# Performance work log

Measured on AMD Instinct MI355X. Metric: run time of the kernel, lower is better.

## Reference

```python
import jax, jax.numpy as jnp
import numpy as np

N = 50000
E = 800000
C_IN = 32
C_OUT = 32
K = 8  # number of branch MLPs


def setup_inputs() -> dict:
    key = jax.random.key(0)
    ks = jax.random.split(key, 12)
    x = jax.random.normal(ks[0], (N, C_IN), dtype=jnp.float32)
    pos = jax.random.normal(ks[1], (N, 2), dtype=jnp.float32)
    edge_index = jax.random.randint(ks[2], (2, E), 0, N, dtype=jnp.int32)
    edge_attr = jax.random.normal(ks[3], (E, 4), dtype=jnp.float32)
    edge_weight = jax.random.uniform(ks[4], (E,), dtype=jnp.float32)
    s1 = 1.0 / np.sqrt(C_IN + 4)
    s2 = 1.0 / np.sqrt(C_OUT)
    W1 = jax.random.uniform(ks[5], (K, C_IN + 4, C_OUT), jnp.float32, -s1, s1)
    b1 = jax.random.uniform(ks[6], (K, C_OUT), jnp.float32, -s1, s1)
    W2 = jax.random.uniform(ks[7], (K, C_OUT, C_OUT), jnp.float32, -s2, s2)
    b2 = jax.random.uniform(ks[8], (K, C_OUT), jnp.float32, -s2, s2)
    sr = 1.0 / np.sqrt(C_IN)
    Wr = jax.random.uniform(ks[9], (C_IN, C_OUT), jnp.float32, -sr, sr)
    br = jax.random.uniform(ks[10], (C_OUT,), jnp.float32, -sr, sr)
    return {"x": x, "pos": pos, "edge_index": edge_index, "edge_attr": edge_attr,
            "edge_weight": edge_weight, "W1": W1, "b1": b1, "W2": W2, "b2": b2,
            "Wr": Wr, "br": br}


def reference(x, pos, edge_index, edge_attr, edge_weight, W1, b1, W2, b2, Wr, br):
    src = edge_index[0]  # j (source / neighbor)
    tgt = edge_index[1]  # i (target / aggregation index)

    # gather per-edge features
    x_i = x[tgt]                      # [E, C_IN]
    x_j = x[src]                      # [E, C_IN]
    diff = pos[src] - pos[tgt]        # [E, 2]

    # geometric branch index in [0, 8)
    con0 = (diff[:, 0] > 0).astype(jnp.int32)
    con1 = (diff[:, 1] > 0).astype(jnp.int32)
    con2 = (jnp.abs(diff[:, 0]) - jnp.abs(diff[:, 1]) > 0).astype(jnp.int32)
    idx = con0 + con1 * 2 + con2 * 4  # [E]

    m = jnp.concatenate([x_j - x_i, edge_attr], axis=1)  # [E, C_IN+4]
    # all 8 branch MLPs (Linear->ReLU->Linear->ReLU), then select per edge
    h = jax.nn.relu(jnp.einsum('ec,kcf->ekf', m, W1) + b1[None])   # [E, K, C_OUT]
    f_all = jax.nn.relu(jnp.einsum('ekf,kfg->ekg', h, W2) + b2[None])
    f = jnp.take_along_axis(f_all, idx[:, None, None], axis=1)[:, 0, :]  # [E, C_OUT]
    f = edge_weight[:, None] * f

    # scatter-mean over target nodes
    seg_sum = jax.ops.segment_sum(f, tgt, num_segments=N)
    counts = jax.ops.segment_sum(jnp.ones((f.shape[0],), f.dtype), tgt, num_segments=N)
    out = seg_sum / jnp.maximum(counts, 1.0)[:, None]

    # skip connection
    out = out + x @ Wr + br
    return out
```

## Files before the change

kernel.cpp:

```cpp
#include <hip/hip_runtime.h>

#define N_NODES 50000
#define N_EDGES 800000
#define K_BR    8
#define BCAP    131072
#define MLP_SLOTS (K_BR * BCAP)
#define SCAN_BLOCKS 196

typedef _Float16 h2 __attribute__((ext_vector_type(2)));
typedef _Float16 half8 __attribute__((ext_vector_type(8)));
typedef float f32x4 __attribute__((ext_vector_type(4)));

#define MFMA(a, b, c) __builtin_amdgcn_mfma_f32_16x16x32_f16((a), (b), (c), 0, 0, 0)

#define VAL_MASK 0x3FFFFFFFu
#define FLG_A    0x40000000u
#define FLG_P    0x80000000u


__device__ __forceinline__ int branch_idx(float dx, float dy) {
    return (dx > 0.0f ? 1 : 0) + (dy > 0.0f ? 2 : 0) +
           ((fabsf(dx) - fabsf(dy)) > 0.0f ? 4 : 0);
}

__device__ __forceinline__ unsigned int pk_bf16(float a, float b) {
    unsigned int ua = __float_as_uint(a), ub = __float_as_uint(b);
    ua += 0x7FFFu + ((ua >> 16) & 1u);
    ub += 0x7FFFu + ((ub >> 16) & 1u);
    return (ua >> 16) | (ub & 0xFFFF0000u);
}

__device__ __forceinline__ unsigned pk_f16pair(float a, float b) {
    h2 p; p.x = (_Float16)a; p.y = (_Float16)b;
    return __builtin_bit_cast(unsigned, p);
}

__device__ __forceinline__ unsigned short f16bits(float a) {
    _Float16 h = (_Float16)a;
    return __builtin_bit_cast(unsigned short, h);
}

__global__ void prep_kernel(const float* __restrict__ W1, const float* __restrict__ W2,
                            const float* __restrict__ x,
                            uint4* __restrict__ w1f4, uint4* __restrict__ w2f4,
                            unsigned* __restrict__ xh) {
    int t = blockIdx.x * 256 + threadIdx.x;
    if (t < 2048) {
        int L = t & 63, fl = t >> 6;
        int nt = fl & 1, kt = (fl >> 1) & 1, k = fl >> 2;
        int quad = L >> 4, col = L & 15;
        unsigned dw[4];
#pragma unroll
        for (int i = 0; i < 4; ++i) {
            float v0 = 0.0f, v1 = 0.0f;
            int k0 = kt * 32 + quad * 8 + 2 * i;
            if (k0 < 36)     v0 = W1[k * 1152 + k0 * 32 + nt * 16 + col];
            if (k0 + 1 < 36) v1 = W1[k * 1152 + (k0 + 1) * 32 + nt * 16 + col];
            dw[i] = pk_f16pair(v0, v1);
        }
        w1f4[t] = make_uint4(dw[0], dw[1], dw[2], dw[3]);
    } else if (t < 3072) {
        int u2 = t - 2048;
        int L = u2 & 63, fl = u2 >> 6;
        int nt = fl & 1, k = fl >> 1;
        int quad = L >> 4, col = L & 15;
        unsigned dw[4];
#pragma unroll
        for (int i = 0; i < 4; ++i) {
            int k0 = quad * 8 + 2 * i;
            dw[i] = pk_f16pair(W2[k * 1024 + k0 * 32 + nt * 16 + col],
                               W2[k * 1024 + (k0 + 1) * 32 + nt * 16 + col]);
        }
        w2f4[u2] = make_uint4(dw[0], dw[1], dw[2], dw[3]);
    }
#pragma unroll
    for (int rep = 0; rep < 2; ++rep) {
        int j = t + rep * 409600;
        if (j < 800000) {
            float2 xv = ((const float2*)x)[j];
            xh[j] = pk_bf16(xv.x, xv.y);
        }
    }
}

__global__ void pass1_kernel(const int* __restrict__ ei, const float* __restrict__ pos,
                             const float* __restrict__ ea, const float* __restrict__ ew,
                             int* __restrict__ cnt, int* __restrict__ bucketCur,
                             uint4* __restrict__ payload) {
    __shared__ int h[K_BR];
    __shared__ int base[K_BR];
    int t = threadIdx.x;
    if (t < K_BR) h[t] = 0;
    __syncthreads();
    int e = blockIdx.x * 256 + t;
    int s = ei[e], d = ei[N_EDGES + e];
    float2 ps = ((const float2*)pos)[s];
    float2 pd = ((const float2*)pos)[d];
    int k = branch_idx(ps.x - pd.x, ps.y - pd.y);
    int rank = atomicAdd(&h[k], 1);
    int slotLocal = atomicAdd(&cnt[d], 1);
    float4 eav = ((const float4*)ea)[e];
    unsigned ewh = (unsigned)f16bits(ew[e]);
    __syncthreads();
    if (t < K_BR) base[t] = (h[t] > 0) ? atomicAdd(&bucketCur[t], h[t]) : 0;
    __syncthreads();
    int idx = (k << 17) + base[k] + rank;
    payload[idx] = make_uint4((unsigned)s | ((unsigned)d << 16),
                              (unsigned)slotLocal | (ewh << 16),
                              pk_f16pair(eav.x, eav.y),
                              pk_f16pair(eav.z, eav.w));
}

__global__ void scan_kernel(const int* __restrict__ cnt, unsigned* __restrict__ ps,
                            int* __restrict__ nodeStart) {
    __shared__ int s[256];
    __shared__ int sh_off;
    int t = threadIdx.x, b = blockIdx.x;
    int i = b * 256 + t;
    int v = (i < N_NODES) ? cnt[i] : 0;
    s[t] = v;
    __syncthreads();
#pragma unroll
    for (int off = 1; off < 256; off <<= 1) {
        int tmp = (t >= off) ? s[t - off] : 0;
        __syncthreads();
        s[t] += tmp;
        __syncthreads();
    }
    int excl = s[t] - v;
    if (t == 255)
        atomicExch(&ps[b], (unsigned)s[255] | (b == 0 ? FLG_P : FLG_A));
    if (t == 0) sh_off = 0;
    if (t < 64 && b > 0) {
        int off = 0;
        int base = b - 1;
        for (;;) {
            int idx = base - t;
            unsigned w = 0;
            if (idx >= 0) {
                do { w = atomicOr(&ps[idx], 0u); } while (!(w & (FLG_A | FLG_P)));
            }
            bool isP = (w & FLG_P) != 0;
            unsigned long long pm = __ballot(isP);
            int firstP = pm ? (__ffsll((unsigned long long)pm) - 1) : 64;
            int contrib = (idx >= 0 && t <= firstP) ? (int)(w & VAL_MASK) : 0;
#pragma unroll
            for (int sh = 32; sh > 0; sh >>= 1) contrib += __shfl_down(contrib, sh, 64);
            contrib = __shfl(contrib, 0, 64);
            off += contrib;
            if (firstP < 64 || base - 64 < 0) break;
            base -= 64;
        }
        if (t == 0) sh_off = off;
    }
    __syncthreads();
    if (i < N_NODES) nodeStart[i] = excl + sh_off;
}

__global__ void __launch_bounds__(128) mlp_kernel(
    const uint4* __restrict__ payload,
    const unsigned* __restrict__ xh,
    const uint4* __restrict__ w1f4, const float* __restrict__ b1,
    const uint4* __restrict__ w2f4, const float* __restrict__ b2,
    const int* __restrict__ nodeStart,
    const int* __restrict__ bucketFill,
    unsigned short* __restrict__ fbuf) {
    __shared__ uint4 lds4[1312];
    char* lds = (char*)lds4;

    int t = blockIdx.x * 128 + threadIdx.x;
    int u = __builtin_amdgcn_readfirstlane(t);
    int k = u >> 17;
    int fill = bucketFill[k];
    if ((u & (BCAP - 1)) >= fill) return;
    int rel = t & (BCAP - 1);
    bool valid = rel < fill;
    int idx = (k << 17) + min(rel, fill - 1);

    int L = threadIdx.x & 63;
    int wv = threadIdx.x >> 6;
    char* mreg = lds + wv * 10496;
    char* hreg = mreg + 9216;
    int quad = L >> 4, col = L & 15;

    uint4 pl = payload[idx];
    int s = (int)(pl.x & 0xFFFFu);
    int d = (int)(pl.x >> 16);
    float w = (float)__builtin_bit_cast(_Float16, (unsigned short)(pl.y >> 16));
    int slot = valid ? (nodeStart[d] + (int)(pl.y & 0xFFFFu)) : 0;

    unsigned mw[16];
    const uint4* xj = ((const uint4*)xh) + 4 * (size_t)s;
    const uint4* xi = ((const uint4*)xh) + 4 * (size_t)d;
#pragma unroll
    for (int q = 0; q < 4; ++q) {
        uint4 a4 = xj[q], b4 = xi[q];
#pragma unroll
        for (int c = 0; c < 4; ++c) {
            unsigned ua = (&a4.x)[c], ub = (&b4.x)[c];
            float d0 = __uint_as_float(ua << 16) - __uint_as_float(ub << 16);
            float d1 = __uint_as_float(ua & 0xFFFF0000u) - __uint_as_float(ub & 0xFFFF0000u);
            mw[4 * q + c] = pk_f16pair(d0, d1);
        }
    }

    uint4* mrow = (uint4*)(mreg + L * 144);
    mrow[0] = make_uint4(mw[0], mw[1], mw[2], mw[3]);
    mrow[1] = make_uint4(mw[4], mw[5], mw[6], mw[7]);
    mrow[2] = make_uint4(mw[8], mw[9], mw[10], mw[11]);
    mrow[3] = make_uint4(mw[12], mw[13], mw[14], mw[15]);
    mrow[4] = make_uint4(pl.z, pl.w, 0u, 0u);
    mrow[5] = make_uint4(0u, 0u, 0u, 0u);
    mrow[6] = make_uint4(0u, 0u, 0u, 0u);
    mrow[7] = make_uint4(0u, 0u, 0u, 0u);

    half8 B1[2][2], B2[2];
#pragma unroll
    for (int kt = 0; kt < 2; ++kt)
#pragma unroll
        for (int nt = 0; nt < 2; ++nt)
            B1[kt][nt] = __builtin_bit_cast(half8, w1f4[((k * 2 + kt) * 2 + nt) * 64 + L]);
#pragma unroll
    for (int nt = 0; nt < 2; ++nt)
        B2[nt] = __builtin_bit_cast(half8, w2f4[(k * 2 + nt) * 64 + L]);
    float b1o0 = b1[k * 32 + col],      b1o1 = b1[k * 32 + 16 + col];
    float b2o0 = b2[k * 32 + col],      b2o1 = b2[k * 32 + 16 + col];

#pragma unroll
    for (int mt = 0; mt < 4; ++mt) {
        int arow = mt * 16 + col;
        half8 a0 = __builtin_bit_cast(half8, *(const uint4*)(mreg + arow * 144 + quad * 16));
        half8 a1 = __builtin_bit_cast(half8, *(const uint4*)(mreg + arow * 144 + 64 + quad * 16));
        f32x4 c0 = {b1o0, b1o0, b1o0, b1o0};
        f32x4 c1 = {b1o1, b1o1, b1o1, b1o1};
        c0 = MFMA(a0, B1[0][0], c0);
        c0 = MFMA(a1, B1[1][0], c0);
        c1 = MFMA(a0, B1[0][1], c1);
        c1 = MFMA(a1, B1[1][1], c1);
#pragma unroll
        for (int r = 0; r < 4; ++r) {
            int er = quad * 4 + r;
            *(unsigned short*)(hreg + er * 80 + col * 2)        = f16bits(fmaxf(c0[r], 0.0f));
            *(unsigned short*)(hreg + er * 80 + (16 + col) * 2) = f16bits(fmaxf(c1[r], 0.0f));
        }
        half8 ah = __builtin_bit_cast(half8, *(const uint4*)(hreg + col * 80 + quad * 16));
        f32x4 d0 = {b2o0, b2o0, b2o0, b2o0};
        f32x4 d1 = {b2o1, b2o1, b2o1, b2o1};
        d0 = MFMA(ah, B2[0], d0);
        d1 = MFMA(ah, B2[1], d1);
#pragma unroll
        for (int r = 0; r < 4; ++r) {
            int edge = mt * 16 + quad * 4 + r;
            *(unsigned short*)(mreg + edge * 144 + col * 2)        = f16bits(fmaxf(d0[r], 0.0f));
            *(unsigned short*)(mreg + edge * 144 + (16 + col) * 2) = f16bits(fmaxf(d1[r], 0.0f));
        }
    }

    uint4* orow = (uint4*)(mreg + L * 144);
    uint4* frow = (uint4*)(fbuf + 32 * (size_t)slot);
#pragma unroll
    for (int q = 0; q < 4; ++q) {
        uint4 v = orow[q];
        unsigned r[4];
#pragma unroll
        for (int c = 0; c < 4; ++c) {
            h2 hv = __builtin_bit_cast(h2, (&v.x)[c]);
            r[c] = pk_bf16((float)hv.x * w, (float)hv.y * w);
        }
        if (valid) frow[q] = make_uint4(r[0], r[1], r[2], r[3]);
    }
}

__global__ void agg_kernel(const unsigned short* __restrict__ fbuf,
                           const int* __restrict__ nodeStart, const int* __restrict__ deg,
                           const float* __restrict__ x, const float* __restrict__ Wr,
                           const float* __restrict__ br, float* __restrict__ out) {
    int t = blockIdx.x * blockDim.x + threadIdx.x;
    if (t >= N_NODES * 8) return;
    int n = t >> 3, g8 = t & 7;
    int st = nodeStart[n], dg = deg[n];
    const uint2* fb = (const uint2*)fbuf;
    float a0 = 0.0f, a1 = 0.0f, a2 = 0.0f, a3 = 0.0f;
    for (int j = 0; j < dg; ++j) {
        uint2 uu = fb[(size_t)(st + j) * 8 + g8];
        a0 += __uint_as_float(uu.x << 16);
        a1 += __uint_as_float(uu.x & 0xFFFF0000u);
        a2 += __uint_as_float(uu.y << 16);
        a3 += __uint_as_float(uu.y & 0xFFFF0000u);
    }
    float inv = 1.0f / (float)max(dg, 1);
    int o = g8 * 4;
    a0 = a0 * inv + br[o];
    a1 = a1 * inv + br[o + 1];
    a2 = a2 * inv + br[o + 2];
    a3 = a3 * inv + br[o + 3];
    const float* xr = x + 32 * (size_t)n;
#pragma unroll
    for (int c = 0; c < 32; ++c) {
        float xv = xr[c];
        a0 = fmaf(xv, Wr[c * 32 + o], a0);
        a1 = fmaf(xv, Wr[c * 32 + o + 1], a1);
        a2 = fmaf(xv, Wr[c * 32 + o + 2], a2);
        a3 = fmaf(xv, Wr[c * 32 + o + 3], a3);
    }
    float4* o4 = (float4*)(out + 32 * (size_t)n + o);
    *o4 = make_float4(a0, a1, a2, a3);
}

extern "C" void kernel_launch(void* const* d_in, const int* in_sizes, int n_in,
                              void* d_out, int out_size, void* d_ws, size_t ws_size,
                              hipStream_t stream) {
    const float* x   = (const float*)d_in[0];
    const float* pos = (const float*)d_in[1];
    const int*   ei  = (const int*)d_in[2];
    const float* ea  = (const float*)d_in[3];
    const float* ew  = (const float*)d_in[4];
    const float* W1  = (const float*)d_in[5];
    const float* b1  = (const float*)d_in[6];
    const float* W2  = (const float*)d_in[7];
    const float* b2  = (const float*)d_in[8];
    const float* Wr  = (const float*)d_in[9];
    const float* br  = (const float*)d_in[10];
    float* out = (float*)d_out;

    char* ws = (char*)d_ws;
    unsigned short* fbuf = (unsigned short*)(ws + 0);
    uint4* payload  = (uint4*)(ws + 51200000);
    int* cnt        = (int*)(ws + 67977216);
    int* bucketCur  = (int*)(ws + 68177216);
    unsigned* psLb  = (unsigned*)(ws + 68177248);
    int* nodeStart  = (int*)(ws + 68178048);
    uint4* w1f4     = (uint4*)(ws + 68378048);
    uint4* w2f4     = (uint4*)(ws + 68410816);
    unsigned* xh    = (unsigned*)(ws + 68427200);

    hipMemsetAsync(cnt, 0, 200832, stream);

    prep_kernel<<<1600, 256, 0, stream>>>(W1, W2, x, w1f4, w2f4, xh);
    pass1_kernel<<<N_EDGES / 256, 256, 0, stream>>>(ei, pos, ea, ew, cnt, bucketCur, payload);
    scan_kernel<<<SCAN_BLOCKS, 256, 0, stream>>>(cnt, psLb, nodeStart);
    mlp_kernel<<<MLP_SLOTS / 128, 128, 0, stream>>>(payload, xh, w1f4, b1, w2f4, b2,
                                                    nodeStart, bucketCur, fbuf);
    agg_kernel<<<(N_NODES * 8 + 255) / 256, 256, 0, stream>>>(fbuf, nodeStart, cnt,
                                                              x, Wr, br, out);
}
```

Measured before the change: 205.4 us.

## Fuse prep into pass1, store x and edge messages in fp16, shrink MLP blocks

Folds the weight-repacking and x conversion work into the edge pass kernel, which removes one kernel launch. x and the per-edge outputs are now stored as fp16 rather than bf16, so the subtraction and edge-weight scaling run as packed half8 vector ops instead of per-element float unpacking and bf16 rounding. The MLP kernel now uses 64-thread single-wave blocks with half the LDS per block, which may let more blocks fit per CU. The trade-offs are a different precision and overflow profile from fp16 in x and f, and an edge-weight multiply done in fp16.

```diff
diff --git a/kernel.cpp b/kernel.cpp
--- a/kernel.cpp
+++ b/kernel.cpp
@@ -23,13 +23,6 @@
            ((fabsf(dx) - fabsf(dy)) > 0.0f ? 4 : 0);
 }
 
-__device__ __forceinline__ unsigned int pk_bf16(float a, float b) {
-    unsigned int ua = __float_as_uint(a), ub = __float_as_uint(b);
-    ua += 0x7FFFu + ((ua >> 16) & 1u);
-    ub += 0x7FFFu + ((ub >> 16) & 1u);
-    return (ua >> 16) | (ub & 0xFFFF0000u);
-}
-
 __device__ __forceinline__ unsigned pk_f16pair(float a, float b) {
     h2 p; p.x = (_Float16)a; p.y = (_Float16)b;
     return __builtin_bit_cast(unsigned, p);
@@ -40,13 +33,24 @@
     return __builtin_bit_cast(unsigned short, h);
 }
 
-__global__ void prep_kernel(const float* __restrict__ W1, const float* __restrict__ W2,
-                            const float* __restrict__ x,
-                            uint4* __restrict__ w1f4, uint4* __restrict__ w2f4,
-                            unsigned* __restrict__ xh) {
-    int t = blockIdx.x * 256 + threadIdx.x;
-    if (t < 2048) {
-        int L = t & 63, fl = t >> 6;
+__global__ void pass1_kernel(const int* __restrict__ ei, const float* __restrict__ pos,
+                             const float* __restrict__ ea, const float* __restrict__ ew,
+                             const float* __restrict__ x,
+                             const float* __restrict__ W1, const float* __restrict__ W2,
+                             int* __restrict__ cnt, int* __restrict__ bucketCur,
+                             uint4* __restrict__ payload, unsigned* __restrict__ xh,
+                             uint4* __restrict__ w1f4, uint4* __restrict__ w2f4) {
+    __shared__ int h[K_BR];
+    __shared__ int base[K_BR];
+    int t = threadIdx.x;
+    int e = blockIdx.x * 256 + t;
+    if (t < K_BR) h[t] = 0;
+
+    float2 xv = ((const float2*)x)[e];
+    xh[e] = pk_f16pair(xv.x, xv.y);
+
+    if (e < 2048) {
+        int L = e & 63, fl = e >> 6;
         int nt = fl & 1, kt = (fl >> 1) & 1, k = fl >> 2;
         int quad = L >> 4, col = L & 15;
         unsigned dw[4];
@@ -58,9 +62,9 @@
             if (k0 + 1 < 36) v1 = W1[k * 1152 + (k0 + 1) * 32 + nt * 16 + col];
             dw[i] = pk_f16pair(v0, v1);
         }
-        w1f4[t] = make_uint4(dw[0], dw[1], dw[2], dw[3]);
-    } else if (t < 3072) {
-        int u2 = t - 2048;
+        w1f4[e] = make_uint4(dw[0], dw[1], dw[2], dw[3]);
+    } else if (e < 3072) {
+        int u2 = e - 2048;
         int L = u2 & 63, fl = u2 >> 6;
         int nt = fl & 1, k = fl >> 1;
         int quad = L >> 4, col = L & 15;
@@ -73,26 +77,8 @@
         }
         w2f4[u2] = make_uint4(dw[0], dw[1], dw[2], dw[3]);
     }
-#pragma unroll
-    for (int rep = 0; rep < 2; ++rep) {
-        int j = t + rep * 409600;
-        if (j < 800000) {
-            float2 xv = ((const float2*)x)[j];
-            xh[j] = pk_bf16(xv.x, xv.y);
-        }
-    }
-}
-
-__global__ void pass1_kernel(const int* __restrict__ ei, const float* __restrict__ pos,
-                             const float* __restrict__ ea, const float* __restrict__ ew,
-                             int* __restrict__ cnt, int* __restrict__ bucketCur,
-                             uint4* __restrict__ payload) {
-    __shared__ int h[K_BR];
-    __shared__ int base[K_BR];
-    int t = threadIdx.x;
-    if (t < K_BR) h[t] = 0;
-    __syncthreads();
-    int e = blockIdx.x * 256 + t;
+
+    __syncthreads();
     int s = ei[e], d = ei[N_EDGES + e];
     float2 ps = ((const float2*)pos)[s];
     float2 pd = ((const float2*)pos)[d];
@@ -157,7 +143,7 @@
     if (i < N_NODES) nodeStart[i] = excl + sh_off;
 }
 
-__global__ void __launch_bounds__(128) mlp_kernel(
+__global__ void __launch_bounds__(64) mlp_kernel(
     const uint4* __restrict__ payload,
     const unsigned* __restrict__ xh,
     const uint4* __restrict__ w1f4, const float* __restrict__ b1,
@@ -165,10 +151,11 @@
     const int* __restrict__ nodeStart,
     const int* __restrict__ bucketFill,
     unsigned short* __restrict__ fbuf) {
-    __shared__ uint4 lds4[1312];
-    char* lds = (char*)lds4;
-
-    int t = blockIdx.x * 128 + threadIdx.x;
+    __shared__ uint4 lds4[656];
+    char* mreg = (char*)lds4;
+    char* hreg = mreg + 9216;
+
+    int t = blockIdx.x * 64 + threadIdx.x;
     int u = __builtin_amdgcn_readfirstlane(t);
     int k = u >> 17;
     int fill = bucketFill[k];
@@ -177,38 +164,25 @@
     bool valid = rel < fill;
     int idx = (k << 17) + min(rel, fill - 1);
 
-    int L = threadIdx.x & 63;
-    int wv = threadIdx.x >> 6;
-    char* mreg = lds + wv * 10496;
-    char* hreg = mreg + 9216;
+    int L = threadIdx.x;
     int quad = L >> 4, col = L & 15;
 
     uint4 pl = payload[idx];
     int s = (int)(pl.x & 0xFFFFu);
     int d = (int)(pl.x >> 16);
-    float w = (float)__builtin_bit_cast(_Float16, (unsigned short)(pl.y >> 16));
+    _Float16 wh = __builtin_bit_cast(_Float16, (unsigned short)(pl.y >> 16));
     int slot = valid ? (nodeStart[d] + (int)(pl.y & 0xFFFFu)) : 0;
 
-    unsigned mw[16];
     const uint4* xj = ((const uint4*)xh) + 4 * (size_t)s;
     const uint4* xi = ((const uint4*)xh) + 4 * (size_t)d;
+    uint4* mrow = (uint4*)(mreg + L * 144);
 #pragma unroll
     for (int q = 0; q < 4; ++q) {
-        uint4 a4 = xj[q], b4 = xi[q];
-#pragma unroll
-        for (int c = 0; c < 4; ++c) {
-            unsigned ua = (&a4.x)[c], ub = (&b4.x)[c];
-            float d0 = __uint_as_float(ua << 16) - __uint_as_float(ub << 16);
-            float d1 = __uint_as_float(ua & 0xFFFF0000u) - __uint_as_float(ub & 0xFFFF0000u);
-            mw[4 * q + c] = pk_f16pair(d0, d1);
-        }
-    }
-
-    uint4* mrow = (uint4*)(mreg + L * 144);
-    mrow[0] = make_uint4(mw[0], mw[1], mw[2], mw[3]);
-    mrow[1] = make_uint4(mw[4], mw[5], mw[6], mw[7]);
-    mrow[2] = make_uint4(mw[8], mw[9], mw[10], mw[11]);
-    mrow[3] = make_uint4(mw[12], mw[13], mw[14], mw[15]);
+        half8 a8 = __builtin_bit_cast(half8, xj[q]);
+        half8 b8 = __builtin_bit_cast(half8, xi[q]);
+        half8 d8 = a8 - b8;
+        mrow[q] = __builtin_bit_cast(uint4, d8);
+    }
     mrow[4] = make_uint4(pl.z, pl.w, 0u, 0u);
     mrow[5] = make_uint4(0u, 0u, 0u, 0u);
     mrow[6] = make_uint4(0u, 0u, 0u, 0u);
@@ -256,18 +230,14 @@
         }
     }
 
+    half8 w8 = {wh, wh, wh, wh, wh, wh, wh, wh};
     uint4* orow = (uint4*)(mreg + L * 144);
     uint4* frow = (uint4*)(fbuf + 32 * (size_t)slot);
 #pragma unroll
     for (int q = 0; q < 4; ++q) {
-        uint4 v = orow[q];
-        unsigned r[4];
-#pragma unroll
-        for (int c = 0; c < 4; ++c) {
-            h2 hv = __builtin_bit_cast(h2, (&v.x)[c]);
-            r[c] = pk_bf16((float)hv.x * w, (float)hv.y * w);
-        }
-        if (valid) frow[q] = make_uint4(r[0], r[1], r[2], r[3]);
+        half8 v8 = __builtin_bit_cast(half8, orow[q]);
+        v8 = v8 * w8;
+        if (valid) frow[q] = __builtin_bit_cast(uint4, v8);
     }
 }
 
@@ -283,10 +253,12 @@
     float a0 = 0.0f, a1 = 0.0f, a2 = 0.0f, a3 = 0.0f;
     for (int j = 0; j < dg; ++j) {
         uint2 uu = fb[(size_t)(st + j) * 8 + g8];
-        a0 += __uint_as_float(uu.x << 16);
-        a1 += __uint_as_float(uu.x & 0xFFFF0000u);
-        a2 += __uint_as_float(uu.y << 16);
-        a3 += __uint_as_float(uu.y & 0xFFFF0000u);
+        h2 p01 = __builtin_bit_cast(h2, uu.x);
+        h2 p23 = __builtin_bit_cast(h2, uu.y);
+        a0 += (float)p01.x;
+        a1 += (float)p01.y;
+        a2 += (float)p23.x;
+        a3 += (float)p23.y;
     }
     float inv = 1.0f / (float)max(dg, 1);
     int o = g8 * 4;
@@ -336,11 +308,12 @@
 
     hipMemsetAsync(cnt, 0, 200832, stream);
 
-    prep_kernel<<<1600, 256, 0, stream>>>(W1, W2, x, w1f4, w2f4, xh);
-    pass1_kernel<<<N_EDGES / 256, 256, 0, stream>>>(ei, pos, ea, ew, cnt, bucketCur, payload);
+    pass1_kernel<<<N_EDGES / 256, 256, 0, stream>>>(ei, pos, ea, ew, x, W1, W2,
+                                                    cnt, bucketCur, payload, xh,
+                                                    w1f4, w2f4);
     scan_kernel<<<SCAN_BLOCKS, 256, 0, stream>>>(cnt, psLb, nodeStart);
-    mlp_kernel<<<MLP_SLOTS / 128, 128, 0, stream>>>(payload, xh, w1f4, b1, w2f4, b2,
-                                                    nodeStart, bucketCur, fbuf);
+    mlp_kernel<<<MLP_SLOTS / 64, 64, 0, stream>>>(payload, xh, w1f4, b1, w2f4, b2,
+                                                  nodeStart, bucketCur, fbuf);
     agg_kernel<<<(N_NODES * 8 + 255) / 256, 256, 0, stream>>>(fbuf, nodeStart, cnt,
                                                               x, Wr, br, out);
 }
```

After: 199.9 us. 2.7% less time.
